# Kernel tuning notes

Measured on AMD Instinct MI355X. Metric: run time of the kernel, lower is better.

Reference implementation:

```python
import jax, jax.numpy as jnp
import numpy as np

H = 16
DH = 64


def setup_inputs() -> dict:
    key = jax.random.key(0)
    ks = jax.random.split(key, 8)
    b, n, m, d = 2, 2048, 2048, 1024
    inner = H * DH  # 1024
    return {
        "x": jax.random.normal(ks[0], (b, n, d), jnp.float32),
        "mem_k": jax.random.normal(ks[1], (b, m, inner), jnp.float32),
        "mem_v": jax.random.normal(ks[2], (b, m, inner), jnp.float32),
        "Wq": jax.random.normal(ks[3], (d, inner), jnp.float32) * (d ** -0.5),
        "Wkv": jax.random.normal(ks[4], (d, 2 * inner), jnp.float32) * (d ** -0.5),
        "b_kv": jax.random.normal(ks[5], (2 * inner,), jnp.float32) * 0.02,
        "Wo": jax.random.normal(ks[6], (inner, d), jnp.float32) * (inner ** -0.5),
        "b_o": jax.random.normal(ks[7], (d,), jnp.float32) * 0.02,
    }


def reference(x, mem_k, mem_v, Wq, Wkv, b_kv, Wo, b_o):
    b, n, d = x.shape
    scale = DH ** -0.5
    q = (x @ Wq) * scale                       # [b, n, h*dh]
    self_k, self_v = jnp.split(x @ Wkv + b_kv, 2, axis=-1)
    k = jnp.concatenate([mem_k, self_k], axis=1)   # [b, j, h*dh]
    v = jnp.concatenate([mem_v, self_v], axis=1)

    def split_heads(t):
        return t.reshape(b, t.shape[1], H, DH).transpose(0, 2, 1, 3)  # b h n d

    q, k, v = map(split_heads, (q, k, v))
    sim = jnp.einsum('bhid,bhjd->bhij', q, k)  # [b, h, n, j]
    i, j = sim.shape[-2:]
    # causal mask: query i may attend to keys up to position (j - i) + i
    causal_mask = jnp.triu(jnp.ones((i, j), dtype=bool), k=j - i + 1)
    mask_value = -jnp.finfo(sim.dtype).max
    sim = jnp.where(causal_mask[None, None], mask_value, sim)
    attn = jax.nn.softmax(sim, axis=-1)
    out = jnp.einsum('bhij,bhjd->bhid', attn, v)
    out = out.transpose(0, 2, 1, 3).reshape(b, n, H * DH)
    return out @ Wo + b_o
```

## Files before the change

kernel.cpp:

```cpp
#include <hip/hip_runtime.h>
#include <stdint.h>

typedef __bf16 bf16x8 __attribute__((ext_vector_type(8)));
typedef _Float16 f16x8 __attribute__((ext_vector_type(8)));
typedef float f32x4 __attribute__((ext_vector_type(4)));
typedef float f32x16 __attribute__((ext_vector_type(16)));

constexpr int Mm = 2048;
constexpr float QSCALE = 0.18033688011112042f;

__device__ __forceinline__ float exp2_fast(float x) {
  return __builtin_amdgcn_exp2f(x);
}

__device__ __forceinline__ uint16_t f2bf(float f) {
  union { float f; uint32_t u; } v; v.f = f;
  return (uint16_t)((v.u + 0x7FFFu + ((v.u >> 16) & 1u)) >> 16);
}
__device__ __forceinline__ uint32_t pack2(float a, float b) {
  return (uint32_t)f2bf(a) | ((uint32_t)f2bf(b) << 16);
}
__device__ __forceinline__ uint32_t pkrtz(float a, float b) {
  auto h2 = __builtin_amdgcn_cvt_pkrtz(a, b);
  return __builtin_bit_cast(uint32_t, h2);
}
__device__ __forceinline__ uint16_t f2h(float f) {
  _Float16 h = (_Float16)f;
  return __builtin_bit_cast(uint16_t, h);
}

__device__ __forceinline__ void async16(const void* g, void* l) {
  __builtin_amdgcn_global_load_lds(
      (__attribute__((address_space(1))) uint32_t*)g,
      (__attribute__((address_space(3))) uint32_t*)l, 16, 0, 0);
}

__device__ __forceinline__ bf16x8 frag64(const uint16_t* base, int row, int chunk) {
  return *(const bf16x8*)(base + row * 64 + chunk * 8);
}
__device__ __forceinline__ f16x8 frag64h(const uint16_t* base, int row, int chunk) {
  return *(const f16x8*)(base + row * 64 + chunk * 8);
}

__global__ __launch_bounds__(256) void prep_kernel(
    const float* __restrict__ x, const float* __restrict__ mem_k,
    const float* __restrict__ mem_v, const float* __restrict__ Wq,
    const float* __restrict__ Wkv, const float* __restrict__ Wo,
    uint16_t* __restrict__ Xb, uint16_t* __restrict__ WallT,
    uint16_t* __restrict__ WoT, uint16_t* __restrict__ Kh,
    uint16_t* __restrict__ VhT) {
  __shared__ float tile[64][65];
  __shared__ uint16_t vtile[64 * 66];
  const int tid = threadIdx.x;
  int blk = blockIdx.x;

  if (blk < 1024) {
    const float4* x4 = (const float4*)x;
    for (int it = 0; it < 4; ++it) {
      int idx4 = blk * 1024 + it * 256 + tid;
      float4 v = x4[idx4];
      uint2 w; w.x = pack2(v.x, v.y); w.y = pack2(v.z, v.w);
      ((uint2*)Xb)[idx4] = w;
    }
    return;
  }
  blk -= 1024;
  if (blk < 1024) {
    const float* src; uint16_t* dst; int ld, colbase, n0, k0;
    if (blk < 768) {
      int nt = blk >> 4, kt = blk & 15;
      n0 = nt * 64; k0 = kt * 64;
      if (n0 < 1024) { src = Wq; ld = 1024; colbase = n0; }
      else           { src = Wkv; ld = 2048; colbase = n0 - 1024; }
      dst = WallT;
    } else {
      int b2 = blk - 768;
      int nt = b2 >> 4, kt = b2 & 15;
      n0 = nt * 64; k0 = kt * 64;
      src = Wo; ld = 1024; colbase = n0; dst = WoT;
    }
    int r = tid >> 4, c = (tid & 15) * 4;
    for (int it = 0; it < 4; ++it) {
      int rr = r + it * 16;
      float4 v = *(const float4*)(src + (size_t)(k0 + rr) * ld + colbase + c);
      tile[rr][c] = v.x; tile[rr][c + 1] = v.y;
      tile[rr][c + 2] = v.z; tile[rr][c + 3] = v.w;
    }
    __syncthreads();
    for (int it = 0; it < 4; ++it) {
      int rn = r + it * 16;
      uint2 w;
      w.x = pack2(tile[c][rn], tile[c + 1][rn]);
      w.y = pack2(tile[c + 2][rn], tile[c + 3][rn]);
      *(uint2*)(dst + (size_t)(n0 + rn) * 1024 + k0 + c) = w;
    }
    return;
  }
  blk -= 1024;
  if (blk < 1024) {
    const float4* s4 = (const float4*)mem_k;
    for (int it = 0; it < 4; ++it) {
      int idx4 = blk * 1024 + it * 256 + tid;
      int e = idx4 * 4;
      int b = e >> 21;
      int rem = e & ((1 << 21) - 1);
      int m = rem >> 10;
      int cc = rem & 1023;
      int h = cc >> 6, dh = cc & 63;
      float4 v = s4[idx4];
      uint2 w; w.x = pack2(v.x, v.y); w.y = pack2(v.z, v.w);
      *(uint2*)(Kh + (((size_t)(b * 16 + h) * 4096) + m) * 64 + dh) = w;
    }
    return;
  }
  blk -= 1024;
  {
    const int b = blk >> 9, h = (blk >> 5) & 15, m0 = (blk & 31) * 64;
    const float4* s4 = (const float4*)mem_v;
    for (int it = 0; it < 4; ++it) {
      int idx = it * 256 + tid;
      int r = idx >> 4, d4 = (idx & 15) * 4;
      float4 v = s4[(size_t)(b * 2048 + m0 + r) * 256 + h * 16 + (d4 >> 2)];
      *(uint32_t*)&vtile[r * 66 + d4]     = pkrtz(v.x, v.y);
      *(uint32_t*)&vtile[r * 66 + d4 + 2] = pkrtz(v.z, v.w);
    }
    __syncthreads();
    for (int it2 = 0; it2 < 2; ++it2) {
      int chunk = it2 * 256 + tid;
      int d = chunk >> 3, mg = chunk & 7;
      uint32_t w[4];
      for (int p = 0; p < 4; ++p) {
        uint32_t lo = vtile[(mg * 8 + 2 * p) * 66 + d];
        uint32_t hi = vtile[(mg * 8 + 2 * p + 1) * 66 + d];
        w[p] = lo | (hi << 16);
      }
      *(uint4*)&VhT[((size_t)((b * 16 + h) * 64) + d) * 4096 + m0 + mg * 8] =
          *(uint4*)w;
    }
  }
}

template <int MODE>
__global__ __launch_bounds__(256) void gemm_kernel(
    const uint16_t* __restrict__ A, const uint16_t* __restrict__ Bt,
    const float* __restrict__ bias, uint16_t* __restrict__ Qh,
    uint16_t* __restrict__ Kh, uint16_t* __restrict__ VhT,
    float* __restrict__ Out) {
  constexpr int K = 1024;
  constexpr int SS = 136;
  constexpr int BM = (MODE == 0) ? 128 : 64;
  constexpr int MT = BM / 32;
  constexpr int CPT = (BM + 128) * 8 / 256;
  const int m0 = blockIdx.x * BM, n0 = blockIdx.y * 128;
  const int tid = threadIdx.x;
  const int wave = tid >> 6, lane = tid & 63;
  const int lhi = lane >> 4, llo = lane & 15;
  const int wm = (wave >> 1) * (BM / 2), wn = (wave & 1) * 64;

  __shared__ uint16_t sh[MODE == 0 ? 128 * SS : (64 + 128) * 64];
  uint16_t* As = sh;
  uint16_t* Bs = sh + BM * 64;

  f32x4 acc[MT][4] = {};

  for (int kt = 0; kt < K / 64; ++kt) {
    __syncthreads();
    for (int c = 0; c < CPT; ++c) {
      int cl = c * 256 + tid;
      if (cl < BM * 8) {
        int row = cl >> 3, ch = cl & 7;
        async16(A + (size_t)(m0 + row) * K + kt * 64 + ch * 8, As + cl * 8);
      } else {
        int bl = cl - BM * 8;
        int row = bl >> 3, ch = bl & 7;
        async16(Bt + (size_t)(n0 + row) * K + kt * 64 + ch * 8, Bs + bl * 8);
      }
    }
    __syncthreads();
    for (int ks = 0; ks < 2; ++ks) {
      bf16x8 af[MT], bfr[4];
      for (int mt = 0; mt < MT; ++mt) af[mt] = frag64(As, wm + mt * 16 + llo, ks * 4 + lhi);
      for (int nt = 0; nt < 4; ++nt) bfr[nt] = frag64(Bs, wn + nt * 16 + llo, ks * 4 + lhi);
      for (int mt = 0; mt < MT; ++mt)
        for (int nt = 0; nt < 4; ++nt)
          acc[mt][nt] = __builtin_amdgcn_mfma_f32_16x16x32_bf16(af[mt], bfr[nt], acc[mt][nt], 0, 0, 0);
    }
  }

  if (MODE == 0) {
    const int region = n0 >> 10;
    __syncthreads();
    for (int nt = 0; nt < 4; ++nt) {
      int cloc = wn + nt * 16 + llo;
      int col = n0 + cloc;
      float badd = (region == 0) ? 0.f : bias[col - 1024];
      for (int mt = 0; mt < 4; ++mt) {
        int rloc = wm + mt * 16 + lhi * 4;
        for (int reg = 0; reg < 4; ++reg) {
          float v = acc[mt][nt][reg];
          v = (region == 0) ? v * QSCALE : v + badd;
          if (region == 2) sh[cloc * SS + rloc + reg] = f2h(v);
          else             sh[(rloc + reg) * SS + cloc] = f2bf(v);
        }
      }
    }
    __syncthreads();
    if (region == 2) {
      const int rl = (tid & 15) * 8;
      for (int it = 0; it < 8; ++it) {
        int cloc = (tid >> 4) + it * 16;
        int col = n0 + cloc;
        int cc = col - 2048, h = cc >> 6, dh = cc & 63;
        int r = m0 + rl;
        int b = r >> 11, n = r & 2047;
        uint4 w = *(const uint4*)&sh[cloc * SS + rl];
        *(uint4*)&VhT[((size_t)((b * 16 + h) * 64) + dh) * 4096 + 2048 + n] = w;
      }
    } else {
      const int cl16 = (tid & 15) * 8;
      const int col = n0 + cl16;
      for (int it = 0; it < 8; ++it) {
        int rloc = (tid >> 4) + it * 16;
        int r = m0 + rloc;
        int b = r >> 11, n = r & 2047;
        uint4 w = *(const uint4*)&sh[rloc * SS + cl16];
        if (region == 0) {
          int h = col >> 6, dh = col & 63;
          *(uint4*)&Qh[(((size_t)(b * 16 + h) * 2048) + n) * 64 + dh] = w;
        } else {
          int cc = col - 1024, h = cc >> 6, dh = cc & 63;
          *(uint4*)&Kh[(((size_t)(b * 16 + h) * 4096) + 2048 + n) * 64 + dh] = w;
        }
      }
    }
  } else {
    for (int nt = 0; nt < 4; ++nt) {
      int col = n0 + wn + nt * 16 + llo;
      float bo = bias[col];
      for (int mt = 0; mt < MT; ++mt) {
        int rbase = m0 + wm + mt * 16 + lhi * 4;
        for (int reg = 0; reg < 4; ++reg)
          Out[(size_t)(rbase + reg) * 1024 + col] = acc[mt][nt][reg] + bo;
      }
    }
  }
}

__global__ __launch_bounds__(256, 2) void attn_kernel(
    const uint16_t* __restrict__ Qh, const uint16_t* __restrict__ Kh,
    const uint16_t* __restrict__ VhT, uint16_t* __restrict__ AO) {
  const int bh = blockIdx.x;
  const int qt = (blockIdx.y < 8) ? (15 - (int)blockIdx.y)
                                  : ((int)blockIdx.y - 8);
  const int tid = threadIdx.x;
  const int wave = tid >> 6, lane = tid & 63;
  const int lo5 = lane & 31, hi = lane >> 5;
  const int qg = wave & 1, kp = wave >> 1;
  const int i0 = qt * 128;
  const int swz5 = lo5 & 7;

  __shared__ uint16_t Ks[2][2][64 * 64];
  __shared__ uint16_t Vt[2][2][64 * 64];

  bf16x8 qf0[4], qf1[4];
  {
    const uint16_t* Qw0 = Qh + ((size_t)bh * 2048 + i0 + qg * 64 + lo5) * 64;
    const uint16_t* Qw1 = Qw0 + 32 * 64;
#pragma unroll
    for (int k = 0; k < 4; ++k) {
      qf0[k] = *(const bf16x8*)(Qw0 + k * 16 + hi * 8);
      qf1[k] = *(const bf16x8*)(Qw1 + k * 16 + hi * 8);
    }
  }

  const uint16_t* Kbh = Kh + (size_t)bh * 4096 * 64;
  const uint16_t* Vbh = VhT + (size_t)bh * 64 * 4096;

  f32x16 o00 = {}, o01 = {}, o10 = {}, o11 = {};
  float l0p = 0.f, l1p = 0.f;

  const int npairs = 17 + qt;

  auto stage = [&](int buf, int u_) {
    const int arr = wave >> 1;
    const int par = wave & 1;
    const int kk0 = u_ * 128 + par * 64;
    uint16_t* dstb = arr == 0 ? &Ks[buf][par][0] : &Vt[buf][par][0];
#pragma unroll
    for (int c = 0; c < 8; ++c) {
      int row = c * 8 + (lane >> 3);
      int chs = (lane & 7) ^ (row & 7);
      const uint16_t* src = arr == 0
          ? Kbh + (size_t)(kk0 + row) * 64 + chs * 8
          : Vbh + (size_t)row * 4096 + kk0 + chs * 8;
      async16(src, dstb + c * 512);
    }
  };

  stage(0, 0);

  const int iw0 = i0 + qg * 64;
  const int iw1 = iw0 + 32;

  for (int u = 0; u < npairs; ++u) {
    const int cur = u & 1;
    __syncthreads();
    if (u + 1 < npairs) stage(cur ^ 1, u + 1);

    const int k0t = (2 * u + kp) * 64;
    const uint16_t* Kt = &Ks[cur][kp][0];
    const uint16_t* Vtt = &Vt[cur][kp][0];

    uint32_t pw0[2][2][4], pw1[2][2][4];

#pragma unroll
    for (int mblk = 0; mblk < 2; ++mblk) {
      f32x16 s0v = {}, s1v = {};
      __builtin_amdgcn_s_setprio(1);
#pragma unroll
      for (int kstep = 0; kstep < 4; ++kstep) {
        bf16x8 kf = frag64(Kt, mblk * 32 + lo5, (2 * kstep + hi) ^ swz5);
        s0v = __builtin_amdgcn_mfma_f32_32x32x16_bf16(kf, qf0[kstep], s0v, 0, 0, 0);
        s1v = __builtin_amdgcn_mfma_f32_32x32x16_bf16(kf, qf1[kstep], s1v, 0, 0, 0);
      }
      __builtin_amdgcn_s_setprio(0);

      if (k0t + mblk * 32 + 31 > Mm + iw0) {
        const int lim = Mm + iw0 + lo5 - k0t - mblk * 32;
#pragma unroll
        for (int r = 0; r < 16; ++r) {
          int kl = (r & 3) + 8 * (r >> 2) + 4 * hi;
          if (kl > lim) s0v[r] = -INFINITY;
        }
      }
      if (k0t + mblk * 32 + 31 > Mm + iw1) {
        const int lim = Mm + iw1 + lo5 - k0t - mblk * 32;
#pragma unroll
        for (int r = 0; r < 16; ++r) {
          int kl = (r & 3) + 8 * (r >> 2) + 4 * hi;
          if (kl > lim) s1v[r] = -INFINITY;
        }
      }

      float e0[16], e1[16];
#pragma unroll
      for (int r = 0; r < 16; ++r) { e0[r] = exp2_fast(s0v[r]); e1[r] = exp2_fast(s1v[r]); }
      {
        float a0 = (e0[0] + e0[1]) + (e0[2] + e0[3]);
        float a1 = (e0[4] + e0[5]) + (e0[6] + e0[7]);
        float a2 = (e0[8] + e0[9]) + (e0[10] + e0[11]);
        float a3 = (e0[12] + e0[13]) + (e0[14] + e0[15]);
        l0p += (a0 + a1) + (a2 + a3);
        float b0 = (e1[0] + e1[1]) + (e1[2] + e1[3]);
        float b1 = (e1[4] + e1[5]) + (e1[6] + e1[7]);
        float b2 = (e1[8] + e1[9]) + (e1[10] + e1[11]);
        float b3 = (e1[12] + e1[13]) + (e1[14] + e1[15]);
        l1p += (b0 + b1) + (b2 + b3);
      }

      uint32_t c0[8], c1[8];
#pragma unroll
      for (int w = 0; w < 8; ++w) {
        c0[w] = pkrtz(e0[2 * w], e0[2 * w + 1]);
        c1[w] = pkrtz(e1[2 * w], e1[2 * w + 1]);
      }
#pragma unroll
      for (int kk2 = 0; kk2 < 2; ++kk2) {
        uint32_t a0 = c0[4 * kk2 + 0], a2 = c0[4 * kk2 + 2];
        uint32_t a1 = c0[4 * kk2 + 1], a3 = c0[4 * kk2 + 3];
        asm volatile("v_permlane32_swap_b32 %0, %1" : "+v"(a0), "+v"(a2));
        asm volatile("v_permlane32_swap_b32 %0, %1" : "+v"(a1), "+v"(a3));
        pw0[mblk][kk2][0] = a0; pw0[mblk][kk2][1] = a1;
        pw0[mblk][kk2][2] = a2; pw0[mblk][kk2][3] = a3;
        uint32_t b0 = c1[4 * kk2 + 0], b2 = c1[4 * kk2 + 2];
        uint32_t b1 = c1[4 * kk2 + 1], b3 = c1[4 * kk2 + 3];
        asm volatile("v_permlane32_swap_b32 %0, %1" : "+v"(b0), "+v"(b2));
        asm volatile("v_permlane32_swap_b32 %0, %1" : "+v"(b1), "+v"(b3));
        pw1[mblk][kk2][0] = b0; pw1[mblk][kk2][1] = b1;
        pw1[mblk][kk2][2] = b2; pw1[mblk][kk2][3] = b3;
      }
    }

#pragma unroll
    for (int mblk = 0; mblk < 2; ++mblk)
#pragma unroll
      for (int kk2 = 0; kk2 < 2; ++kk2) {
        const int kk = mblk * 2 + kk2;
        uint4 fwa; fwa.x = pw0[mblk][kk2][0]; fwa.y = pw0[mblk][kk2][1];
        fwa.z = pw0[mblk][kk2][2]; fwa.w = pw0[mblk][kk2][3];
        f16x8 pa0 = __builtin_bit_cast(f16x8, fwa);
        uint4 fwb; fwb.x = pw1[mblk][kk2][0]; fwb.y = pw1[mblk][kk2][1];
        fwb.z = pw1[mblk][kk2][2]; fwb.w = pw1[mblk][kk2][3];
        f16x8 pa1 = __builtin_bit_cast(f16x8, fwb);
        f16x8 vf0 = frag64h(Vtt, lo5,      (2 * kk + hi) ^ swz5);
        f16x8 vf1 = frag64h(Vtt, 32 + lo5, (2 * kk + hi) ^ swz5);
        __builtin_amdgcn_s_setprio(1);
        o00 = __builtin_amdgcn_mfma_f32_32x32x16_f16(pa0, vf0, o00, 0, 0, 0);
        o01 = __builtin_amdgcn_mfma_f32_32x32x16_f16(pa0, vf1, o01, 0, 0, 0);
        o10 = __builtin_amdgcn_mfma_f32_32x32x16_f16(pa1, vf0, o10, 0, 0, 0);
        o11 = __builtin_amdgcn_mfma_f32_32x32x16_f16(pa1, vf1, o11, 0, 0, 0);
        __builtin_amdgcn_s_setprio(0);
      }
  }

  float l0full, l1full;
  {
    float a0 = l0p, b0 = l0p;
    asm volatile("v_permlane32_swap_b32 %0, %1" : "+v"(a0), "+v"(b0));
    l0full = a0 + b0;
    float a1 = l1p, b1 = l1p;
    asm volatile("v_permlane32_swap_b32 %0, %1" : "+v"(a1), "+v"(b1));
    l1full = a1 + b1;
  }

  const int b = bh >> 4, h = bh & 15;
  float* F = (float*)&Ks[0][0][0];
  float* L = (float*)&Vt[1][0][0];
  uint16_t* Es = &Vt[0][0][0];

  __syncthreads();
  if (hi == 0) {
    L[kp * 128 + qg * 64 + lo5]      = l0full;
    L[kp * 128 + qg * 64 + 32 + lo5] = l1full;
  }
  if (kp == 1) {
#pragma unroll
    for (int r = 0; r < 16; ++r) {
      int q0 = qg * 64 + (r & 3) + 8 * (r >> 2) + 4 * hi;
      int q1 = q0 + 32;
      F[q0 * 64 + lo5]      = o00[r];
      F[q0 * 64 + 32 + lo5] = o01[r];
      F[q1 * 64 + lo5]      = o10[r];
      F[q1 * 64 + 32 + lo5] = o11[r];
    }
  }
  __syncthreads();
  if (kp == 0) {
#pragma unroll
    for (int r = 0; r < 16; ++r) {
      int q0 = qg * 64 + (r & 3) + 8 * (r >> 2) + 4 * hi;
      int q1 = q0 + 32;
      float inv0 = 1.0f / (L[q0] + L[128 + q0]);
      float inv1 = 1.0f / (L[q1] + L[128 + q1]);
      Es[q0 * 64 + lo5]      = f2bf((o00[r] + F[q0 * 64 + lo5]) * inv0);
      Es[q0 * 64 + 32 + lo5] = f2bf((o01[r] + F[q0 * 64 + 32 + lo5]) * inv0);
      Es[q1 * 64 + lo5]      = f2bf((o10[r] + F[q1 * 64 + lo5]) * inv1);
      Es[q1 * 64 + 32 + lo5] = f2bf((o11[r] + F[q1 * 64 + 32 + lo5]) * inv1);
    }
  }
  __syncthreads();
  {
    int row = tid >> 1, c32 = (tid & 1) * 32;
    size_t base = ((size_t)(b * 2048) + i0 + row) * 1024 + h * 64 + c32;
    *(uint4*)&AO[base]      = *(const uint4*)&Es[row * 64 + c32];
    *(uint4*)&AO[base + 8]  = *(const uint4*)&Es[row * 64 + c32 + 8];
    *(uint4*)&AO[base + 16] = *(const uint4*)&Es[row * 64 + c32 + 16];
    *(uint4*)&AO[base + 24] = *(const uint4*)&Es[row * 64 + c32 + 24];
  }
}

extern "C" void kernel_launch(void* const* d_in, const int* in_sizes, int n_in,
                              void* d_out, int out_size, void* d_ws,
                              size_t ws_size, hipStream_t stream) {
  const float* x     = (const float*)d_in[0];
  const float* mem_k = (const float*)d_in[1];
  const float* mem_v = (const float*)d_in[2];
  const float* Wq    = (const float*)d_in[3];
  const float* Wkv   = (const float*)d_in[4];
  const float* b_kv  = (const float*)d_in[5];
  const float* Wo    = (const float*)d_in[6];
  const float* b_o   = (const float*)d_in[7];
  float* out = (float*)d_out;

  char* ws = (char*)d_ws;
  uint16_t* Xb    = (uint16_t*)(ws);
  uint16_t* WallT = (uint16_t*)(ws + (8ull << 20));
  uint16_t* WoT   = (uint16_t*)(ws + (14ull << 20));
  uint16_t* Qh    = (uint16_t*)(ws + (16ull << 20));
  uint16_t* Kh    = (uint16_t*)(ws + (24ull << 20));
  uint16_t* VhT   = (uint16_t*)(ws + (40ull << 20));
  uint16_t* AO    = (uint16_t*)(ws + (56ull << 20));

  prep_kernel<<<4096, 256, 0, stream>>>(x, mem_k, mem_v, Wq, Wkv, Wo,
                                        Xb, WallT, WoT, Kh, VhT);
  gemm_kernel<0><<<dim3(32, 24), 256, 0, stream>>>(Xb, WallT, b_kv,
                                                   Qh, Kh, VhT, nullptr);
  attn_kernel<<<dim3(32, 16), 256, 0, stream>>>(Qh, Kh, VhT, AO);
  gemm_kernel<1><<<dim3(64, 8), 256, 0, stream>>>(AO, WoT, b_o,
                                                  nullptr, nullptr, nullptr, out);
}
```

Measured before the change: 236.8 us.

## Software-pipeline PV MFMAs into the next tile's QK phase

Defers each tile's P·V MFMAs to the following loop iteration, issuing them right after the first QK MFMA block. The aim is to overlap the exp/softmax VALU work with matrix-core work. V fragments are preloaded into registers, and the P fragments stay live across iterations. A final drain after the loop handles the last tile. The exp, sum and pack loop is also fused into one pass. The cost is higher VGPR pressure, which could reduce occupancy or cause spills.

```diff
diff --git a/kernel.cpp b/kernel.cpp
--- a/kernel.cpp
+++ b/kernel.cpp
@@ -302,6 +302,9 @@
   const int iw0 = i0 + qg * 64;
   const int iw1 = iw0 + 32;
 
+  uint32_t pw0[2][2][4], pw1[2][2][4];
+  f16x8 vfr[8];
+
   for (int u = 0; u < npairs; ++u) {
     const int cur = u & 1;
     __syncthreads();
@@ -310,8 +313,6 @@
     const int k0t = (2 * u + kp) * 64;
     const uint16_t* Kt = &Ks[cur][kp][0];
     const uint16_t* Vtt = &Vt[cur][kp][0];
-
-    uint32_t pw0[2][2][4], pw1[2][2][4];
 
 #pragma unroll
     for (int mblk = 0; mblk < 2; ++mblk) {
@@ -325,6 +326,34 @@
       }
       __builtin_amdgcn_s_setprio(0);
 
+      if (mblk == 0) {
+        if (u > 0) {
+          __builtin_amdgcn_s_setprio(1);
+#pragma unroll
+          for (int pm = 0; pm < 2; ++pm)
+#pragma unroll
+            for (int kk2 = 0; kk2 < 2; ++kk2) {
+              const int kk = pm * 2 + kk2;
+              uint4 fwa; fwa.x = pw0[pm][kk2][0]; fwa.y = pw0[pm][kk2][1];
+              fwa.z = pw0[pm][kk2][2]; fwa.w = pw0[pm][kk2][3];
+              f16x8 pa0 = __builtin_bit_cast(f16x8, fwa);
+              uint4 fwb; fwb.x = pw1[pm][kk2][0]; fwb.y = pw1[pm][kk2][1];
+              fwb.z = pw1[pm][kk2][2]; fwb.w = pw1[pm][kk2][3];
+              f16x8 pa1 = __builtin_bit_cast(f16x8, fwb);
+              o00 = __builtin_amdgcn_mfma_f32_32x32x16_f16(pa0, vfr[2 * kk + 0], o00, 0, 0, 0);
+              o01 = __builtin_amdgcn_mfma_f32_32x32x16_f16(pa0, vfr[2 * kk + 1], o01, 0, 0, 0);
+              o10 = __builtin_amdgcn_mfma_f32_32x32x16_f16(pa1, vfr[2 * kk + 0], o10, 0, 0, 0);
+              o11 = __builtin_amdgcn_mfma_f32_32x32x16_f16(pa1, vfr[2 * kk + 1], o11, 0, 0, 0);
+            }
+          __builtin_amdgcn_s_setprio(0);
+        }
+#pragma unroll
+        for (int kk = 0; kk < 4; ++kk) {
+          vfr[2 * kk + 0] = frag64h(Vtt, lo5,      (2 * kk + hi) ^ swz5);
+          vfr[2 * kk + 1] = frag64h(Vtt, 32 + lo5, (2 * kk + hi) ^ swz5);
+        }
+      }
+
       if (k0t + mblk * 32 + 31 > Mm + iw0) {
         const int lim = Mm + iw0 + lo5 - k0t - mblk * 32;
 #pragma unroll
@@ -342,27 +371,15 @@
         }
       }
 
-      float e0[16], e1[16];
-#pragma unroll
-      for (int r = 0; r < 16; ++r) { e0[r] = exp2_fast(s0v[r]); e1[r] = exp2_fast(s1v[r]); }
-      {
-        float a0 = (e0[0] + e0[1]) + (e0[2] + e0[3]);
-        float a1 = (e0[4] + e0[5]) + (e0[6] + e0[7]);
-        float a2 = (e0[8] + e0[9]) + (e0[10] + e0[11]);
-        float a3 = (e0[12] + e0[13]) + (e0[14] + e0[15]);
-        l0p += (a0 + a1) + (a2 + a3);
-        float b0 = (e1[0] + e1[1]) + (e1[2] + e1[3]);
-        float b1 = (e1[4] + e1[5]) + (e1[6] + e1[7]);
-        float b2 = (e1[8] + e1[9]) + (e1[10] + e1[11]);
-        float b3 = (e1[12] + e1[13]) + (e1[14] + e1[15]);
-        l1p += (b0 + b1) + (b2 + b3);
-      }
-
       uint32_t c0[8], c1[8];
 #pragma unroll
       for (int w = 0; w < 8; ++w) {
-        c0[w] = pkrtz(e0[2 * w], e0[2 * w + 1]);
-        c1[w] = pkrtz(e1[2 * w], e1[2 * w + 1]);
+        float a0 = exp2_fast(s0v[2 * w]), a1 = exp2_fast(s0v[2 * w + 1]);
+        c0[w] = pkrtz(a0, a1);
+        l0p += a0 + a1;
+        float b0 = exp2_fast(s1v[2 * w]), b1 = exp2_fast(s1v[2 * w + 1]);
+        c1[w] = pkrtz(b0, b1);
+        l1p += b0 + b1;
       }
 #pragma unroll
       for (int kk2 = 0; kk2 < 2; ++kk2) {
@@ -380,28 +397,26 @@
         pw1[mblk][kk2][2] = b2; pw1[mblk][kk2][3] = b3;
       }
     }
-
-#pragma unroll
-    for (int mblk = 0; mblk < 2; ++mblk)
-#pragma unroll
-      for (int kk2 = 0; kk2 < 2; ++kk2) {
-        const int kk = mblk * 2 + kk2;
-        uint4 fwa; fwa.x = pw0[mblk][kk2][0]; fwa.y = pw0[mblk][kk2][1];
-        fwa.z = pw0[mblk][kk2][2]; fwa.w = pw0[mblk][kk2][3];
-        f16x8 pa0 = __builtin_bit_cast(f16x8, fwa);
-        uint4 fwb; fwb.x = pw1[mblk][kk2][0]; fwb.y = pw1[mblk][kk2][1];
-        fwb.z = pw1[mblk][kk2][2]; fwb.w = pw1[mblk][kk2][3];
-        f16x8 pa1 = __builtin_bit_cast(f16x8, fwb);
-        f16x8 vf0 = frag64h(Vtt, lo5,      (2 * kk + hi) ^ swz5);
-        f16x8 vf1 = frag64h(Vtt, 32 + lo5, (2 * kk + hi) ^ swz5);
-        __builtin_amdgcn_s_setprio(1);
-        o00 = __builtin_amdgcn_mfma_f32_32x32x16_f16(pa0, vf0, o00, 0, 0, 0);
-        o01 = __builtin_amdgcn_mfma_f32_32x32x16_f16(pa0, vf1, o01, 0, 0, 0);
-        o10 = __builtin_amdgcn_mfma_f32_32x32x16_f16(pa1, vf0, o10, 0, 0, 0);
-        o11 = __builtin_amdgcn_mfma_f32_32x32x16_f16(pa1, vf1, o11, 0, 0, 0);
-        __builtin_amdgcn_s_setprio(0);
-      }
-  }
+  }
+
+  __builtin_amdgcn_s_setprio(1);
+#pragma unroll
+  for (int pm = 0; pm < 2; ++pm)
+#pragma unroll
+    for (int kk2 = 0; kk2 < 2; ++kk2) {
+      const int kk = pm * 2 + kk2;
+      uint4 fwa; fwa.x = pw0[pm][kk2][0]; fwa.y = pw0[pm][kk2][1];
+      fwa.z = pw0[pm][kk2][2]; fwa.w = pw0[pm][kk2][3];
+      f16x8 pa0 = __builtin_bit_cast(f16x8, fwa);
+      uint4 fwb; fwb.x = pw1[pm][kk2][0]; fwb.y = pw1[pm][kk2][1];
+      fwb.z = pw1[pm][kk2][2]; fwb.w = pw1[pm][kk2][3];
+      f16x8 pa1 = __builtin_bit_cast(f16x8, fwb);
+      o00 = __builtin_amdgcn_mfma_f32_32x32x16_f16(pa0, vfr[2 * kk + 0], o00, 0, 0, 0);
+      o01 = __builtin_amdgcn_mfma_f32_32x32x16_f16(pa0, vfr[2 * kk + 1], o01, 0, 0, 0);
+      o10 = __builtin_amdgcn_mfma_f32_32x32x16_f16(pa1, vfr[2 * kk + 0], o10, 0, 0, 0);
+      o11 = __builtin_amdgcn_mfma_f32_32x32x16_f16(pa1, vfr[2 * kk + 1], o11, 0, 0, 0);
+    }
+  __builtin_amdgcn_s_setprio(0);
 
   float l0full, l1full;
   {
```

Result: slower. 273.4 us (+15.5%).
